# Kernel tuning notes

Hardware: AMD Instinct MI355X
Metric: run time of the kernel (lower is better)

The kernel has to match this reference:

```python
import jax, jax.numpy as jnp
import numpy as np

B, S, D, H = 2, 4096, 768, 12
HD = D // H
SCALE = HD ** -0.5


def setup_inputs() -> dict:
    key = jax.random.key(0)
    k_x, k_wq, k_bq, k_wp, k_bp = jax.random.split(key, 5)
    lim_qkv = (1.0 / D) ** 0.5
    lim_p = (1.0 / D) ** 0.5
    return {
        "x": jax.random.normal(k_x, (B, S, D), dtype=jnp.float32),
        "qkv_w": jax.random.uniform(k_wq, (3 * D, D), dtype=jnp.float32, minval=-lim_qkv, maxval=lim_qkv),
        "qkv_b": jax.random.uniform(k_bq, (3 * D,), dtype=jnp.float32, minval=-lim_qkv, maxval=lim_qkv),
        "proj_w": jax.random.uniform(k_wp, (D, D), dtype=jnp.float32, minval=-lim_p, maxval=lim_p),
        "proj_b": jax.random.uniform(k_bp, (D,), dtype=jnp.float32, minval=-lim_p, maxval=lim_p),
    }


def reference(x, qkv_w, qkv_b, proj_w, proj_b):
    b, s, _ = x.shape
    qkv = x @ qkv_w.T + qkv_b                      # [b, s, 3D]
    q, k, v = jnp.split(qkv, 3, axis=-1)           # each [b, s, D]
    # [b, s, D] -> [b, H, s, HD]
    def to_heads(t):
        return t.reshape(b, s, H, HD).transpose(0, 2, 1, 3)
    q, k, v = to_heads(q), to_heads(k), to_heads(v)
    attn = jnp.einsum("bhqd,bhkd->bhqk", q, k) * SCALE   # [b, H, s, s]
    attn = jax.nn.softmax(attn, axis=-1)
    out = jnp.einsum("bhqk,bhkd->bhqd", attn, v)         # [b, H, s, HD]
    out = out.transpose(0, 2, 1, 3).reshape(b, s, D)
    return out @ proj_w.T + proj_b
```

## Files before the change

### kernel.cpp

```cpp
#include <hip/hip_runtime.h>
#include <hip/hip_bf16.h>


#define B_ 2
#define S_ 4096
#define D_ 768
#define H_ 12
#define HD_ 64
#define TD_ (3 * D_)
#define QKD_ (2 * D_)

static constexpr float LOG2E = 1.4426950408889634f;

typedef __bf16 bf16x8 __attribute__((ext_vector_type(8)));
typedef unsigned short ushortx8 __attribute__((ext_vector_type(8)));
typedef unsigned short ushortx4 __attribute__((ext_vector_type(4)));
typedef float floatx4 __attribute__((ext_vector_type(4)));

__device__ inline unsigned short f2bf(float f) {
  return __builtin_bit_cast(unsigned short, (__bf16)f);
}
__device__ inline float bf2f(unsigned short u) {
  return __uint_as_float(((unsigned int)u) << 16);
}
__device__ inline void glds16(const unsigned short* g, unsigned short* l) {
  __builtin_amdgcn_global_load_lds(
      (const __attribute__((address_space(1))) unsigned int*)g,
      (__attribute__((address_space(3))) unsigned int*)l, 16, 0, 0);
}

__global__ __launch_bounds__(256)
void cvt_bf16(const float* __restrict__ src, unsigned short* __restrict__ dst, int n4) {
  int idx = blockIdx.x * 256 + threadIdx.x;
  if (idx < n4) {
    floatx4 v = *reinterpret_cast<const floatx4*>(&src[(size_t)idx * 4]);
    ushortx4 o;
#pragma unroll
    for (int j = 0; j < 4; ++j) o[j] = f2bf(v[j]);
    *reinterpret_cast<ushortx4*>(&dst[(size_t)idx * 4]) = o;
  }
}

template <int NFR, bool QKV_EPI>
__global__ __launch_bounds__(256)
void gemm_bf16(const unsigned short* __restrict__ A,
               const unsigned short* __restrict__ W,
               const float* __restrict__ bias,
               float* __restrict__ Cf,
               unsigned short* __restrict__ qkbuf,
               unsigned short* __restrict__ vT,
               int M, int N, int K) {
  constexpr int BM = 128, BN = NFR * 32, BK = 64;
  __shared__ __attribute__((aligned(16))) unsigned short As[BM][BK];
  __shared__ __attribute__((aligned(16))) unsigned short Ws[BN][BK];

  const int tid = threadIdx.x;
  const int lane = tid & 63;
  const int wid = tid >> 6;
  const int wm = wid >> 1;
  const int wn = wid & 1;
  const int m0 = blockIdx.y * BM;
  const int n0 = blockIdx.x * BN;
  const int lr = lane & 15;
  const int g = lane >> 4;
  const int e8 = lr & 7;
  const int ro = g * 4;
  const int srow = lane >> 3;
  const int sch = lane & 7;

  floatx4 acc[4][NFR];
#pragma unroll
  for (int m = 0; m < 4; ++m)
#pragma unroll
    for (int n = 0; n < NFR; ++n) acc[m][n] = (floatx4){0.f, 0.f, 0.f, 0.f};

  for (int kb = 0; kb < K; kb += BK) {
#pragma unroll
    for (int c = 0; c < 4; ++c) {
      int seg = wid * 4 + c;
      int row = seg * 8 + srow;
      glds16(&A[(size_t)(m0 + row) * K + kb + ((sch ^ srow) << 3)], &As[seg * 8][0]);
    }
#pragma unroll
    for (int c = 0; c < NFR; ++c) {
      int seg = wid * NFR + c;
      int row = seg * 8 + srow;
      glds16(&W[(size_t)(n0 + row) * K + kb + ((sch ^ srow) << 3)], &Ws[seg * 8][0]);
    }
    __syncthreads();

#pragma unroll
    for (int ks = 0; ks < 2; ++ks) {
      int ch = ((ks << 2) + g) ^ e8;
      bf16x8 af[4], bfr[NFR];
#pragma unroll
      for (int m = 0; m < 4; ++m)
        af[m] = *reinterpret_cast<const bf16x8*>(&As[wm * 64 + m * 16 + lr][ch << 3]);
#pragma unroll
      for (int n = 0; n < NFR; ++n)
        bfr[n] = *reinterpret_cast<const bf16x8*>(&Ws[wn * (NFR * 16) + n * 16 + lr][ch << 3]);
#pragma unroll
      for (int m = 0; m < 4; ++m)
#pragma unroll
        for (int n = 0; n < NFR; ++n)
          acc[m][n] = __builtin_amdgcn_mfma_f32_16x16x32_bf16(af[m], bfr[n], acc[m][n], 0, 0, 0);
    }
    __syncthreads();
  }

#pragma unroll
  for (int n = 0; n < NFR; ++n) {
    int col = n0 + wn * (NFR * 16) + n * 16 + lr;
    float bv = bias[col];
#pragma unroll
    for (int m = 0; m < 4; ++m) {
      int row = m0 + wm * 64 + m * 16 + ro;
      if constexpr (QKV_EPI) {
        if (col >= QKD_) {
          int dcol = col - QKD_;
          int hh = dcol >> 6, dd = dcol & 63;
          int bb = row >> 12, s = row & (S_ - 1);
          int s5 = s & 31;
          int spos = (s & ~31) + ((s5 >> 2) & 3) * 8 + ((s5 >> 4) & 1) * 4;
          ushortx4 o4;
#pragma unroll
          for (int i = 0; i < 4; ++i) o4[i] = f2bf(acc[m][n][i] + bv);
          *reinterpret_cast<ushortx4*>(
              &vT[(size_t)((bb * H_ + hh) * 64 + dd) * S_ + spos]) = o4;
        } else {
#pragma unroll
          for (int i = 0; i < 4; ++i)
            qkbuf[(size_t)(row + i) * QKD_ + col] = f2bf(acc[m][n][i] + bv);
        }
      } else {
#pragma unroll
        for (int i = 0; i < 4; ++i)
          Cf[(size_t)(row + i) * N + col] = acc[m][n][i] + bv;
      }
    }
  }
}

template <int NSPLIT>
__global__ __launch_bounds__(256)
void attn_kernel(const unsigned short* __restrict__ qkbuf,
                 const unsigned short* __restrict__ vT,
                 unsigned short* __restrict__ outb,
                 float* __restrict__ po, float* __restrict__ pl) {
  constexpr int QB = 128, KVB = 64, NT = S_ / KVB / NSPLIT;
  __shared__ __attribute__((aligned(16))) unsigned short Ks[2][KVB][64];
  __shared__ __attribute__((aligned(16))) unsigned short Vt[2][HD_][64];

  const int tid = threadIdx.x;
  const int lane = tid & 63;
  const int wid = tid >> 6;
  const int q0 = blockIdx.x * QB;
  const int h = blockIdx.y;
  const int b = (NSPLIT == 1) ? blockIdx.z : (blockIdx.z >> 1);
  const int sp = (NSPLIT == 1) ? 0 : (blockIdx.z & 1);
  const int kvbase = sp * (S_ / NSPLIT);
  const int lr = lane & 15;
  const int g = lane >> 4;
  const int e8 = lr & 7;
  const int wq = wid * 32;

  const unsigned short* Qg = qkbuf + (size_t)b * S_ * QKD_ + (size_t)h * HD_;
  const unsigned short* Kg = Qg + D_;
  const unsigned short* Vg = vT + (size_t)(b * H_ + h) * HD_ * S_;

  const int srow = lane >> 3;
  const int sch = lane & 7;

  bf16x8 qf[2][2];
#pragma unroll
  for (int qt = 0; qt < 2; ++qt)
#pragma unroll
    for (int ks = 0; ks < 2; ++ks) {
      ushortx8 r = *reinterpret_cast<const ushortx8*>(
          &Qg[(size_t)(q0 + wq + qt * 16 + lr) * QKD_ + ks * 32 + g * 8]);
      bf16x8 q;
#pragma unroll
      for (int j = 0; j < 8; ++j) q[j] = (__bf16)(bf2f(r[j]) * (0.125f * LOG2E));
      qf[qt][ks] = q;
    }

  floatx4 lrv[2] = {(floatx4){0.f, 0.f, 0.f, 0.f}, (floatx4){0.f, 0.f, 0.f, 0.f}};
  floatx4 oacc[2][4];
#pragma unroll
  for (int qt = 0; qt < 2; ++qt)
#pragma unroll
    for (int dt = 0; dt < 4; ++dt) oacc[qt][dt] = (floatx4){0.f, 0.f, 0.f, 0.f};

  const unsigned short* kp0 = Kg + (size_t)(kvbase + wid * 16 + srow) * QKD_ + ((sch ^ srow) << 3);
  const unsigned short* kp1 = kp0 + (size_t)8 * QKD_;
  const unsigned short* vp0 = Vg + (size_t)(wid * 16 + srow) * S_ + kvbase + ((sch ^ srow) << 3);
  const unsigned short* vp1 = vp0 + (size_t)8 * S_;

#define STAGE(BUF) do { \
    glds16(kp0, &Ks[BUF][wid * 16][0]); \
    glds16(kp1, &Ks[BUF][wid * 16 + 8][0]); \
    glds16(vp0, &Vt[BUF][wid * 16][0]); \
    glds16(vp1, &Vt[BUF][wid * 16 + 8][0]); \
    kp0 += (size_t)KVB * QKD_; kp1 += (size_t)KVB * QKD_; \
    vp0 += KVB; vp1 += KVB; } while (0)

#define COMPUTE(BUF) do { \
    bf16x8 kf[4][2], vf[2][4]; \
    _Pragma("unroll") \
    for (int kt = 0; kt < 4; ++kt) \
      _Pragma("unroll") \
      for (int ks = 0; ks < 2; ++ks) \
        kf[kt][ks] = *reinterpret_cast<const bf16x8*>( \
            &Ks[BUF][kt * 16 + lr][(((ks << 2) + g) ^ e8) * 8]); \
    _Pragma("unroll") \
    for (int ks = 0; ks < 2; ++ks) \
      _Pragma("unroll") \
      for (int dt = 0; dt < 4; ++dt) \
        vf[ks][dt] = *reinterpret_cast<const bf16x8*>( \
            &Vt[BUF][dt * 16 + lr][(((ks << 2) + g) ^ e8) * 8]); \
    _Pragma("unroll") \
    for (int qt = 0; qt < 2; ++qt) { \
      floatx4 sc[4]; \
      _Pragma("unroll") \
      for (int kt = 0; kt < 4; ++kt) { \
        floatx4 c = (floatx4){0.f, 0.f, 0.f, 0.f}; \
        _Pragma("unroll") \
        for (int ks = 0; ks < 2; ++ks) \
          c = __builtin_amdgcn_mfma_f32_16x16x32_bf16(kf[kt][ks], qf[qt][ks], c, 0, 0, 0); \
        sc[kt] = c; \
      } \
      _Pragma("unroll") \
      for (int kt = 0; kt < 4; ++kt) \
        _Pragma("unroll") \
        for (int i = 0; i < 4; ++i) \
          sc[kt][i] = __builtin_amdgcn_exp2f(sc[kt][i]); \
      lrv[qt] += (sc[0] + sc[1]) + (sc[2] + sc[3]); \
      bf16x8 pf0, pf1; \
      _Pragma("unroll") \
      for (int j = 0; j < 8; ++j) { \
        pf0[j] = (__bf16)sc[(j >> 2)][j & 3]; \
        pf1[j] = (__bf16)sc[2 + (j >> 2)][j & 3]; \
      } \
      _Pragma("unroll") \
      for (int dt = 0; dt < 4; ++dt) \
        oacc[qt][dt] = __builtin_amdgcn_mfma_f32_16x16x32_bf16(vf[0][dt], pf0, oacc[qt][dt], 0, 0, 0); \
      _Pragma("unroll") \
      for (int dt = 0; dt < 4; ++dt) \
        oacc[qt][dt] = __builtin_amdgcn_mfma_f32_16x16x32_bf16(vf[1][dt], pf1, oacc[qt][dt], 0, 0, 0); \
    } } while (0)

  STAGE(0);
  for (int t = 0; t < NT; t += 2) {
    __syncthreads();
    STAGE(1);
    COMPUTE(0);
    __syncthreads();
    if (t + 2 < NT) STAGE(0);
    COMPUTE(1);
  }
#undef STAGE
#undef COMPUTE

#pragma unroll
  for (int qt = 0; qt < 2; ++qt) {
    float l = (lrv[qt][0] + lrv[qt][1]) + (lrv[qt][2] + lrv[qt][3]);
    l += __shfl_xor(l, 16, 64);
    l += __shfl_xor(l, 32, 64);
    int q = q0 + wq + qt * 16 + lr;
    if constexpr (NSPLIT == 1) {
      float inv = __builtin_amdgcn_rcpf(l);
      size_t rowbase = ((size_t)b * S_ + q) * D_ + h * HD_;
#pragma unroll
      for (int dt = 0; dt < 4; ++dt) {
        ushortx4 o4;
#pragma unroll
        for (int i = 0; i < 4; ++i) o4[i] = f2bf(oacc[qt][dt][i] * inv);
        *reinterpret_cast<ushortx4*>(&outb[rowbase + dt * 16 + 4 * g]) = o4;
      }
    } else {
      size_t rowbase = ((size_t)(sp * B_ + b) * S_ + q) * D_ + h * HD_;
#pragma unroll
      for (int dt = 0; dt < 4; ++dt)
        *reinterpret_cast<floatx4*>(&po[rowbase + dt * 16 + 4 * g]) = oacc[qt][dt];
      if (lane < 16)
        pl[((size_t)((sp * B_ + b) * H_ + h)) * S_ + q] = l;
    }
  }
}

__global__ __launch_bounds__(256)
void combine_kernel(const float* __restrict__ po, const float* __restrict__ pl,
                    unsigned short* __restrict__ attnbuf) {
  int gid = blockIdx.x * 256 + threadIdx.x;
  int d4 = gid & 15;
  int rest = gid >> 4;
  int h = rest % H_;
  int bq = rest / H_;
  size_t o0 = (size_t)bq * D_ + h * 64 + d4 * 4;
  const size_t half = (size_t)B_ * S_ * D_;
  floatx4 a = *reinterpret_cast<const floatx4*>(&po[o0]);
  floatx4 c = *reinterpret_cast<const floatx4*>(&po[o0 + half]);
  int q = bq & (S_ - 1);
  int b = bq >> 12;
  float l = pl[(size_t)(b * H_ + h) * S_ + q] +
            pl[(size_t)((B_ + b) * H_ + h) * S_ + q];
  float inv = __builtin_amdgcn_rcpf(l);
  ushortx4 o;
#pragma unroll
  for (int i = 0; i < 4; ++i) o[i] = f2bf((a[i] + c[i]) * inv);
  *reinterpret_cast<ushortx4*>(&attnbuf[o0]) = o;
}

extern "C" void kernel_launch(void* const* d_in, const int* in_sizes, int n_in,
                              void* d_out, int out_size, void* d_ws, size_t ws_size,
                              hipStream_t stream) {
  const float* x      = (const float*)d_in[0];
  const float* qkv_w  = (const float*)d_in[1];
  const float* qkv_b  = (const float*)d_in[2];
  const float* proj_w = (const float*)d_in[3];
  const float* proj_b = (const float*)d_in[4];
  float* out = (float*)d_out;

  unsigned short* qkbuf   = (unsigned short*)d_ws;
  unsigned short* vTbuf   = qkbuf + (size_t)B_ * S_ * QKD_;
  unsigned short* attnbuf = vTbuf + (size_t)B_ * H_ * HD_ * S_;
  unsigned short* xbf     = attnbuf + (size_t)B_ * S_ * D_;
  unsigned short* wqkvbf  = xbf + (size_t)B_ * S_ * D_;
  unsigned short* wprojbf = wqkvbf + (size_t)TD_ * D_;
  float* po = (float*)(wprojbf + (size_t)D_ * D_);
  float* pl = po + (size_t)2 * B_ * S_ * D_;

  const size_t need = ((char*)(pl + (size_t)2 * B_ * H_ * S_)) - (char*)d_ws;
  const bool split = ws_size >= need;

  dim3 blk(256);
  cvt_bf16<<<dim3((B_ * S_ * D_ / 4 + 255) / 256), blk, 0, stream>>>(x, xbf, B_ * S_ * D_ / 4);
  cvt_bf16<<<dim3((TD_ * D_ / 4 + 255) / 256), blk, 0, stream>>>(qkv_w, wqkvbf, TD_ * D_ / 4);
  cvt_bf16<<<dim3((D_ * D_ / 4 + 255) / 256), blk, 0, stream>>>(proj_w, wprojbf, D_ * D_ / 4);

  gemm_bf16<4, true><<<dim3(TD_ / 128, (B_ * S_) / 128), blk, 0, stream>>>(
      xbf, wqkvbf, qkv_b, nullptr, qkbuf, vTbuf, B_ * S_, TD_, D_);

  if (split) {
    attn_kernel<2><<<dim3(S_ / 128, H_, B_ * 2), blk, 0, stream>>>(
        qkbuf, vTbuf, attnbuf, po, pl);
    combine_kernel<<<dim3(B_ * S_ * H_ * 16 / 256), blk, 0, stream>>>(po, pl, attnbuf);
  } else {
    attn_kernel<1><<<dim3(S_ / 128, H_, B_), blk, 0, stream>>>(
        qkbuf, vTbuf, attnbuf, nullptr, nullptr);
  }

  gemm_bf16<2, false><<<dim3(D_ / 64, (B_ * S_) / 128), blk, 0, stream>>>(
      attnbuf, wprojbf, proj_b, out, nullptr, nullptr, B_ * S_, D_, D_);
}
```

Before: 216.2 us.

## Compute softmax row sums via MFMA with ones and flatten LDS addressing

```diff
diff --git a/kernel.cpp b/kernel.cpp
--- a/kernel.cpp
+++ b/kernel.cpp
@@ -148,8 +148,7 @@
                  unsigned short* __restrict__ outb,
                  float* __restrict__ po, float* __restrict__ pl) {
   constexpr int QB = 128, KVB = 64, NT = S_ / KVB / NSPLIT;
-  __shared__ __attribute__((aligned(16))) unsigned short Ks[2][KVB][64];
-  __shared__ __attribute__((aligned(16))) unsigned short Vt[2][HD_][64];
+  __shared__ __attribute__((aligned(16))) unsigned short L[2 * 8192];
 
   const int tid = threadIdx.x;
   const int lane = tid & 63;
@@ -184,12 +183,28 @@
       qf[qt][ks] = q;
     }
 
-  floatx4 lrv[2] = {(floatx4){0.f, 0.f, 0.f, 0.f}, (floatx4){0.f, 0.f, 0.f, 0.f}};
+  bf16x8 onesf;
+#pragma unroll
+  for (int j = 0; j < 8; ++j) onesf[j] = (__bf16)1.0f;
+
+  floatx4 lacc[2] = {(floatx4){0.f, 0.f, 0.f, 0.f}, (floatx4){0.f, 0.f, 0.f, 0.f}};
   floatx4 oacc[2][4];
 #pragma unroll
   for (int qt = 0; qt < 2; ++qt)
 #pragma unroll
     for (int dt = 0; dt < 4; ++dt) oacc[qt][dt] = (floatx4){0.f, 0.f, 0.f, 0.f};
+
+  int koff[4][2], voff[2][4];
+#pragma unroll
+  for (int kt = 0; kt < 4; ++kt)
+#pragma unroll
+    for (int ks = 0; ks < 2; ++ks)
+      koff[kt][ks] = (kt * 16 + lr) * 64 + ((((ks << 2) + g) ^ e8) << 3);
+#pragma unroll
+  for (int ks = 0; ks < 2; ++ks)
+#pragma unroll
+    for (int dt = 0; dt < 4; ++dt)
+      voff[ks][dt] = 4096 + (dt * 16 + lr) * 64 + ((((ks << 2) + g) ^ e8) << 3);
 
   const unsigned short* kp0 = Kg + (size_t)(kvbase + wid * 16 + srow) * QKD_ + ((sch ^ srow) << 3);
   const unsigned short* kp1 = kp0 + (size_t)8 * QKD_;
@@ -197,10 +212,10 @@
   const unsigned short* vp1 = vp0 + (size_t)8 * S_;
 
 #define STAGE(BUF) do { \
-    glds16(kp0, &Ks[BUF][wid * 16][0]); \
-    glds16(kp1, &Ks[BUF][wid * 16 + 8][0]); \
-    glds16(vp0, &Vt[BUF][wid * 16][0]); \
-    glds16(vp1, &Vt[BUF][wid * 16 + 8][0]); \
+    glds16(kp0, &L[(BUF) * 8192 + (wid * 16) * 64]); \
+    glds16(kp1, &L[(BUF) * 8192 + (wid * 16 + 8) * 64]); \
+    glds16(vp0, &L[(BUF) * 8192 + 4096 + (wid * 16) * 64]); \
+    glds16(vp1, &L[(BUF) * 8192 + 4096 + (wid * 16 + 8) * 64]); \
     kp0 += (size_t)KVB * QKD_; kp1 += (size_t)KVB * QKD_; \
     vp0 += KVB; vp1 += KVB; } while (0)
 
@@ -210,14 +225,12 @@
     for (int kt = 0; kt < 4; ++kt) \
       _Pragma("unroll") \
       for (int ks = 0; ks < 2; ++ks) \
-        kf[kt][ks] = *reinterpret_cast<const bf16x8*>( \
-            &Ks[BUF][kt * 16 + lr][(((ks << 2) + g) ^ e8) * 8]); \
+        kf[kt][ks] = *reinterpret_cast<const bf16x8*>(&L[(BUF) * 8192 + koff[kt][ks]]); \
     _Pragma("unroll") \
     for (int ks = 0; ks < 2; ++ks) \
       _Pragma("unroll") \
       for (int dt = 0; dt < 4; ++dt) \
-        vf[ks][dt] = *reinterpret_cast<const bf16x8*>( \
-            &Vt[BUF][dt * 16 + lr][(((ks << 2) + g) ^ e8) * 8]); \
+        vf[ks][dt] = *reinterpret_cast<const bf16x8*>(&L[(BUF) * 8192 + voff[ks][dt]]); \
     _Pragma("unroll") \
     for (int qt = 0; qt < 2; ++qt) { \
       floatx4 sc[4]; \
@@ -234,13 +247,14 @@
         _Pragma("unroll") \
         for (int i = 0; i < 4; ++i) \
           sc[kt][i] = __builtin_amdgcn_exp2f(sc[kt][i]); \
-      lrv[qt] += (sc[0] + sc[1]) + (sc[2] + sc[3]); \
       bf16x8 pf0, pf1; \
       _Pragma("unroll") \
       for (int j = 0; j < 8; ++j) { \
         pf0[j] = (__bf16)sc[(j >> 2)][j & 3]; \
         pf1[j] = (__bf16)sc[2 + (j >> 2)][j & 3]; \
       } \
+      lacc[qt] = __builtin_amdgcn_mfma_f32_16x16x32_bf16(onesf, pf0, lacc[qt], 0, 0, 0); \
+      lacc[qt] = __builtin_amdgcn_mfma_f32_16x16x32_bf16(onesf, pf1, lacc[qt], 0, 0, 0); \
       _Pragma("unroll") \
       for (int dt = 0; dt < 4; ++dt) \
         oacc[qt][dt] = __builtin_amdgcn_mfma_f32_16x16x32_bf16(vf[0][dt], pf0, oacc[qt][dt], 0, 0, 0); \
@@ -263,9 +277,7 @@
 
 #pragma unroll
   for (int qt = 0; qt < 2; ++qt) {
-    float l = (lrv[qt][0] + lrv[qt][1]) + (lrv[qt][2] + lrv[qt][3]);
-    l += __shfl_xor(l, 16, 64);
-    l += __shfl_xor(l, 32, 64);
+    float l = lacc[qt][0];
     int q = q0 + wq + qt * 16 + lr;
     if constexpr (NSPLIT == 1) {
       float inv = __builtin_amdgcn_rcpf(l);
```

Measured after the change: 201.0 us. 7.0% less time.
